# Kernel tuning notes

Measured on AMD Instinct MI355X. Metric: run time of the kernel, lower is better.

The kernel has to match this reference:

```python
import jax, jax.numpy as jnp
import numpy as np


def setup_inputs() -> dict:
    key = jax.random.key(0)
    k1, k2 = jax.random.split(key)
    B, N, G = 16, 200000, 128
    velocity = jax.random.normal(k1, (B, 3, G, G, G), dtype=jnp.float32)
    points = jax.random.uniform(k2, (B, N, 3), dtype=jnp.float32, minval=-2.5, maxval=2.5)
    bounding_box = jnp.array([[-2.5, 2.5], [-2.5, 2.5], [-2.5, 2.5]], dtype=jnp.float32)
    return {"velocity": velocity, "points": points, "bounding_box": bounding_box, "grid_size": G}


def reference(velocity, points, bounding_box, grid_size):
    # velocity: [B, 3, G, G, G]; points: [B, N, 3]; bounding_box: [3, 2]
    B, N, dim = points.shape
    G = grid_size
    # permute channels last and flatten grid, matching torch .permute(0,2,3,4,1).view(B,-1,3)
    vel = jnp.transpose(velocity, (0, 2, 3, 4, 1)).reshape(B, G * G * G, dim)
    bb = bounding_box
    # map points into continuous grid coordinates, per-axis
    uvw = (points - bb[:, 0]) / (bb[:, 1] - bb[:, 0]) * (G - 1)  # [B, N, 3]
    f1 = jnp.clip(jnp.floor(jax.lax.stop_gradient(uvw)), 0, G - 1)
    frac = uvw - f1          # fu, fv, fw
    gfrac = f1 + 1.0 - uvw   # gu, gv, gw
    i1 = f1.astype(jnp.int32)                      # floor indices (clamped)
    i2 = jnp.clip(i1 + 1, 0, G - 1)                # ceil indices (clamped)

    def gather(idx):  # idx: [B, N] -> [B, N, 3]
        return jax.vmap(lambda v, i: v[i])(vel, idx)

    out = jnp.zeros((B, N, dim), dtype=velocity.dtype)
    # 8 trilinear corners
    for iu, wu in ((i1[..., 0], gfrac[..., 0]), (i2[..., 0], frac[..., 0])):
        for iv, wv in ((i1[..., 1], gfrac[..., 1]), (i2[..., 1], frac[..., 1])):
            for iw, ww in ((i1[..., 2], gfrac[..., 2]), (i2[..., 2], frac[..., 2])):
                idx = (iu * G + iv) * G + iw
                out = out + gather(idx) * (wu * wv * ww)[..., None]
    return out
```

## Files before the change

kernel.cpp:

```cpp
#include <hip/hip_runtime.h>
#include <hip/hip_fp16.h>


constexpr int G = 128;
constexpr long long G3 = (long long)G * G * G;
constexpr int NSLAB = 8;
constexpr int NBU = 32, NBV = 32;
constexpr int NBIN = NBU * NBV;
constexpr int WINPTS = 4096;
constexpr int NIT = WINPTS / 256;
constexpr int MAXWIN = 64;

__global__ __launch_bounds__(256) void bin_kernel(
    const float* __restrict__ pts,
    const float* __restrict__ bb,
    int* __restrict__ Pt,
    unsigned long long* __restrict__ payload,
    int N, int nwin)
{
    __shared__ int hist[NBIN];
    __shared__ int psum[256];

    int b = blockIdx.x / nwin;
    int w = blockIdx.x % nwin;
    for (int i = threadIdx.x; i < NBIN; i += 256) hist[i] = 0;
    __syncthreads();

    const float Gm1 = (float)(G - 1);
    float bx0 = bb[0], bx1 = bb[1];
    float by0 = bb[2], by1 = bb[3];
    float bz0 = bb[4], bz1 = bb[5];
    long long pbase = (long long)b * N;
    int n0 = w * WINPTS;

    unsigned long long qc[NIT];
    #pragma unroll
    for (int it = 0; it < NIT; ++it) {
        int n = n0 + it * 256 + threadIdx.x;
        qc[it] = ~0ull;
        if (n < N) {
            const float* p = pts + (pbase + n) * 3;
            float u  = (p[0] - bx0) / (bx1 - bx0) * Gm1;
            float v  = (p[1] - by0) / (by1 - by0) * Gm1;
            float wz = (p[2] - bz0) / (bz1 - bz0) * Gm1;
            u  = fminf(fmaxf(u, 0.f), Gm1);
            v  = fminf(fmaxf(v, 0.f), Gm1);
            wz = fminf(fmaxf(wz, 0.f), Gm1);
            unsigned int qu = (unsigned int)(u * 1024.0f);
            unsigned int qv = (unsigned int)(v * 1024.0f);
            unsigned int qw = (unsigned int)(wz * 1024.0f);
            int nl = n - n0;
            qc[it] = (unsigned long long)qu
                   | ((unsigned long long)qv << 17)
                   | ((unsigned long long)qw << 34)
                   | ((unsigned long long)nl << 51);
            atomicAdd(&hist[((qu >> 12) << 5) | (qv >> 12)], 1);
        }
    }
    __syncthreads();

    int t = threadIdx.x;
    int l0 = hist[4 * t], l1 = hist[4 * t + 1], l2 = hist[4 * t + 2], l3 = hist[4 * t + 3];
    int s = l0 + l1 + l2 + l3;
    psum[t] = s;
    __syncthreads();
    for (int off = 1; off < 256; off <<= 1) {
        int v = (t >= off) ? psum[t - off] : 0;
        __syncthreads();
        psum[t] += v;
        __syncthreads();
    }
    int run = psum[t] - s;

    long long prow = ((long long)b * NBIN + 4 * t) * nwin + w;
    Pt[prow]            = run; hist[4 * t]     = run; run += l0;
    Pt[prow + nwin]     = run; hist[4 * t + 1] = run; run += l1;
    Pt[prow + 2 * nwin] = run; hist[4 * t + 2] = run; run += l2;
    Pt[prow + 3 * nwin] = run; hist[4 * t + 3] = run; run += l3;
    __syncthreads();

    unsigned long long* seg = payload + (long long)(b * nwin + w) * WINPTS;
    #pragma unroll
    for (int it = 0; it < NIT; ++it) {
        unsigned long long q = qc[it];
        if (q != ~0ull) {
            unsigned int qu = (unsigned int)(q & 0x1FFFF);
            unsigned int qv = (unsigned int)((q >> 17) & 0x1FFFF);
            int bin = ((qu >> 12) << 5) | (qv >> 12);
            int pos = atomicAdd(&hist[bin], 1);
            seg[pos] = q;
        }
    }
}

__global__ __launch_bounds__(256) void trilerp_lds_kernel(
    const float* __restrict__ vel,
    const int* __restrict__ Pt,
    const unsigned long long* __restrict__ payload,
    float* __restrict__ out,
    int N, int nwin)
{
    __shared__ unsigned short s_h[3 * 25 * 128];
    __shared__ int loc[MAXWIN];
    __shared__ int sc[MAXWIN];

    int x = blockIdx.x;
    int slab = x & (NSLAB - 1);
    int rest = x >> 3;
    int b    = rest >> 7;
    int r2   = rest & 127;
    int iu4  = (slab << 2) | (r2 >> 5);
    int iv4  = r2 & 31;
    int binLocal = (iu4 << 5) | iv4;
    long long lin = (long long)b * NBIN + binLocal;

    int tid = threadIdx.x;
    if (tid < nwin) {
        int l  = Pt[lin * nwin + tid];
        int nl = (binLocal < NBIN - 1) ? Pt[(lin + 1) * nwin + tid]
                                       : min(WINPTS, N - tid * WINPTS);
        loc[tid] = l;
        sc[tid]  = nl - l;
    } else if (tid < MAXWIN) {
        loc[tid] = 0; sc[tid] = 0;
    }

    int u0 = iu4 << 2, v0 = iv4 << 2;
    for (int k = 0; k < 10; ++k) {
        int idx = tid + k * 256;
        if (idx < 2400) {
            int f4 = idx & 31;
            int ru = idx >> 5;
            int ch = ru / 25;
            int r  = ru - ch * 25;
            int gu = min(u0 + r / 5, G - 1);
            int gv = min(v0 + (r - (r / 5) * 5), G - 1);
            long long src = (((long long)b * 3 + ch) << 21) + ((long long)gu << 14) + (gv << 7) + (f4 << 2);
            float4 val = *reinterpret_cast<const float4*>(vel + src);
            unsigned int lo32 = (unsigned int)__half_as_ushort(__float2half(val.x))
                              | ((unsigned int)__half_as_ushort(__float2half(val.y)) << 16);
            unsigned int hi32 = (unsigned int)__half_as_ushort(__float2half(val.z))
                              | ((unsigned int)__half_as_ushort(__float2half(val.w)) << 16);
            *reinterpret_cast<uint2*>(&s_h[((ch * 25 + r) << 7) + (f4 << 2)]) = make_uint2(lo32, hi32);
        }
    }
    __syncthreads();

    for (int off = 1; off < MAXWIN; off <<= 1) {
        int v = 0;
        if (tid < MAXWIN && tid >= off) v = sc[tid - off];
        __syncthreads();
        if (tid < MAXWIN) sc[tid] += v;
        __syncthreads();
    }
    int total = sc[nwin - 1];
    const float Gm1 = (float)(G - 1);
    const float INV1024 = 1.0f / 1024.0f;

    auto h2f = [](unsigned short us) -> float {
        return __half2float(__ushort_as_half(us));
    };

    for (int i = tid; i < total; i += 256) {
        int lo2 = 0, hi2 = nwin - 1;
        while (lo2 < hi2) { int mid = (lo2 + hi2) >> 1; if (sc[mid] > i) hi2 = mid; else lo2 = mid + 1; }
        int w = lo2;
        int excl = (w == 0) ? 0 : sc[w - 1];
        long long pidx = (long long)(b * nwin + w) * WINPTS + loc[w] + (i - excl);
        unsigned long long q = payload[pidx];
        unsigned int qu = (unsigned int)(q & 0x1FFFF);
        unsigned int qv = (unsigned int)((q >> 17) & 0x1FFFF);
        unsigned int qw = (unsigned int)((q >> 34) & 0x1FFFF);
        int nl = (int)(q >> 51);
        int t = (int)((long long)b * N + w * WINPTS + nl);

        float u  = (float)qu * INV1024;
        float v  = (float)qv * INV1024;
        float wq = (float)qw * INV1024;

        float fu = floorf(u);
        float fv = floorf(v);
        float fw = floorf(wq);

        float du = u - fu, dv = v - fv, dw = wq - fw;
        float gu = fu + 1.0f - u;
        float gv = fv + 1.0f - v;
        float gw = fw + 1.0f - wq;

        int iu1 = (int)fu, iv1 = (int)fv, iw1 = (int)fw;
        int iu2 = min(iu1 + 1, G - 1);
        int iv2 = min(iv1 + 1, G - 1);
        int iwb = min(iw1, G - 2);
        bool lo = (iw1 <= G - 2);

        float w11 = gu * gv, w12 = gu * dv, w21 = du * gv, w22 = du * dv;

        int du1 = iu1 - u0, dv1 = iv1 - v0;
        int du2 = iu2 - u0, dv2 = iv2 - v0;

        float o[3];
        #pragma unroll
        for (int ch = 0; ch < 3; ++ch) {
            int rb = ch * 25;
            int b11 = (rb + du1 * 5 + dv1) << 7;
            int b12 = (rb + du1 * 5 + dv2) << 7;
            int b21 = (rb + du2 * 5 + dv1) << 7;
            int b22 = (rb + du2 * 5 + dv2) << 7;
            float l11 = h2f(s_h[b11 + iwb]), h11 = h2f(s_h[b11 + iwb + 1]);
            float l12 = h2f(s_h[b12 + iwb]), h12 = h2f(s_h[b12 + iwb + 1]);
            float l21 = h2f(s_h[b21 + iwb]), h21 = h2f(s_h[b21 + iwb + 1]);
            float l22 = h2f(s_h[b22 + iwb]), h22 = h2f(s_h[b22 + iwb + 1]);
            float a11 = lo ? l11 : h11;
            float a12 = lo ? l12 : h12;
            float a21 = lo ? l21 : h21;
            float a22 = lo ? l22 : h22;
            o[ch] = w11 * (gw * a11 + dw * h11)
                  + w12 * (gw * a12 + dw * h12)
                  + w21 * (gw * a21 + dw * h21)
                  + w22 * (gw * a22 + dw * h22);
        }

        float* op = out + (long long)t * 3;
        op[0] = o[0]; op[1] = o[1]; op[2] = o[2];
    }
}

__global__ __launch_bounds__(256) void trilerp_pair_kernel(
    const float* __restrict__ vel, const float* __restrict__ pts,
    const float* __restrict__ bb, float* __restrict__ out,
    int N, int nchunk)
{
    int bid  = blockIdx.x;
    int slab = bid & (NSLAB - 1);
    int t    = bid >> 3;
    int c    = t % nchunk;
    int b    = t / nchunk;
    int n = c * 256 + threadIdx.x;
    if (n >= N) return;

    float bx0 = bb[0], bx1 = bb[1];
    float by0 = bb[2], by1 = bb[3];
    float bz0 = bb[4], bz1 = bb[5];
    long long pi = (long long)b * N + n;
    const float* p = pts + pi * 3;
    float px = p[0], py = p[1], pz = p[2];
    const float Gm1 = (float)(G - 1);
    float u = (px - bx0) / (bx1 - bx0) * Gm1;
    float fu = fminf(fmaxf(floorf(u), 0.f), Gm1);
    int iu1 = (int)fu;
    if ((iu1 >> 4) != slab) return;
    float v = (py - by0) / (by1 - by0) * Gm1;
    float w = (pz - bz0) / (bz1 - bz0) * Gm1;
    float fv = fminf(fmaxf(floorf(v), 0.f), Gm1);
    float fw = fminf(fmaxf(floorf(w), 0.f), Gm1);
    float du = u - fu, dv = v - fv, dw = w - fw;
    float gu = fu + 1.0f - u, gv = fv + 1.0f - v, gw = fw + 1.0f - w;
    int iv1 = (int)fv, iw1 = (int)fw;
    int iu2 = min(iu1 + 1, G - 1);
    int iv2 = min(iv1 + 1, G - 1);
    int iwb = min(iw1, G - 2);
    bool lo = (iw1 <= G - 2);
    float w11 = gu * gv, w12 = gu * dv, w21 = du * gv, w22 = du * dv;
    const float* vb = vel + (long long)b * 3 * G3;
    long long o11 = (long long)((iu1 << 7) + iv1) * G + iwb;
    long long o12 = (long long)((iu1 << 7) + iv2) * G + iwb;
    long long o21 = (long long)((iu2 << 7) + iv1) * G + iwb;
    long long o22 = (long long)((iu2 << 7) + iv2) * G + iwb;
    float o[3];
    #pragma unroll
    for (int chn = 0; chn < 3; ++chn) {
        const float* vc = vb + (long long)chn * G3;
        float2 p11 = *reinterpret_cast<const float2*>(vc + o11);
        float2 p12 = *reinterpret_cast<const float2*>(vc + o12);
        float2 p21 = *reinterpret_cast<const float2*>(vc + o21);
        float2 p22 = *reinterpret_cast<const float2*>(vc + o22);
        float a11 = lo ? p11.x : p11.y;
        float a12 = lo ? p12.x : p12.y;
        float a21 = lo ? p21.x : p21.y;
        float a22 = lo ? p22.x : p22.y;
        o[chn] = w11 * (gw * a11 + dw * p11.y)
               + w12 * (gw * a12 + dw * p12.y)
               + w21 * (gw * a21 + dw * p21.y)
               + w22 * (gw * a22 + dw * p22.y);
    }
    float* op = out + pi * 3;
    op[0] = o[0]; op[1] = o[1]; op[2] = o[2];
}

extern "C" void kernel_launch(void* const* d_in, const int* in_sizes, int n_in,
                              void* d_out, int out_size, void* d_ws, size_t ws_size,
                              hipStream_t stream) {
    const float* vel = (const float*)d_in[0];
    const float* pts = (const float*)d_in[1];
    const float* bb  = (const float*)d_in[2];
    float* out = (float*)d_out;

    int B = (int)(in_sizes[0] / (3 * G3));
    int N = in_sizes[1] / (3 * B);
    int nwin = (N + WINPTS - 1) / WINPTS;

    auto align256 = [](size_t x) { return (x + 255) & ~(size_t)255; };
    size_t off_pt  = 0;
    size_t sz_pt   = (size_t)B * NBIN * nwin * 4;
    size_t off_pay = align256(off_pt + sz_pt);
    size_t sz_pay  = (size_t)B * nwin * WINPTS * 8;
    size_t need    = off_pay + sz_pay;

    if (ws_size >= need && nwin <= MAXWIN) {
        int* Pt = (int*)((char*)d_ws + off_pt);
        unsigned long long* payload = (unsigned long long*)((char*)d_ws + off_pay);

        bin_kernel<<<B * nwin, 256, 0, stream>>>(pts, bb, Pt, payload, N, nwin);
        trilerp_lds_kernel<<<B * NBIN, 256, 0, stream>>>(vel, Pt, payload, out, N, nwin);
    } else {
        int nchunk = (N + 255) / 256;
        long long blocks = (long long)B * nchunk * NSLAB;
        trilerp_pair_kernel<<<(int)blocks, 256, 0, stream>>>(vel, pts, bb, out, N, nchunk);
    }
}
```

Measured before the change: 165.8 us.

## Split spatial bins along w axis into two halves with smaller LDS tiles

```diff
diff --git a/kernel.cpp b/kernel.cpp
--- a/kernel.cpp
+++ b/kernel.cpp
@@ -5,11 +5,11 @@
 constexpr int G = 128;
 constexpr long long G3 = (long long)G * G * G;
 constexpr int NSLAB = 8;
-constexpr int NBU = 32, NBV = 32;
-constexpr int NBIN = NBU * NBV;
+constexpr int NBIN = 2048;
 constexpr int WINPTS = 4096;
 constexpr int NIT = WINPTS / 256;
 constexpr int MAXWIN = 64;
+constexpr int WROW = 68;
 
 __global__ __launch_bounds__(256) void bin_kernel(
     const float* __restrict__ pts,
@@ -54,14 +54,16 @@
                    | ((unsigned long long)qv << 17)
                    | ((unsigned long long)qw << 34)
                    | ((unsigned long long)nl << 51);
-            atomicAdd(&hist[((qu >> 12) << 5) | (qv >> 12)], 1);
+            int bin = ((qu >> 12) << 6) | (((qv >> 12)) << 1) | (qw >> 16);
+            atomicAdd(&hist[bin], 1);
         }
     }
     __syncthreads();
 
     int t = threadIdx.x;
-    int l0 = hist[4 * t], l1 = hist[4 * t + 1], l2 = hist[4 * t + 2], l3 = hist[4 * t + 3];
-    int s = l0 + l1 + l2 + l3;
+    int l[8], s = 0;
+    #pragma unroll
+    for (int j = 0; j < 8; ++j) { l[j] = hist[8 * t + j]; s += l[j]; }
     psum[t] = s;
     __syncthreads();
     for (int off = 1; off < 256; off <<= 1) {
@@ -72,11 +74,13 @@
     }
     int run = psum[t] - s;
 
-    long long prow = ((long long)b * NBIN + 4 * t) * nwin + w;
-    Pt[prow]            = run; hist[4 * t]     = run; run += l0;
-    Pt[prow + nwin]     = run; hist[4 * t + 1] = run; run += l1;
-    Pt[prow + 2 * nwin] = run; hist[4 * t + 2] = run; run += l2;
-    Pt[prow + 3 * nwin] = run; hist[4 * t + 3] = run; run += l3;
+    long long prow = ((long long)b * NBIN + 8 * t) * nwin + w;
+    #pragma unroll
+    for (int j = 0; j < 8; ++j) {
+        Pt[prow + (long long)j * nwin] = run;
+        hist[8 * t + j] = run;
+        run += l[j];
+    }
     __syncthreads();
 
     unsigned long long* seg = payload + (long long)(b * nwin + w) * WINPTS;
@@ -86,32 +90,34 @@
         if (q != ~0ull) {
             unsigned int qu = (unsigned int)(q & 0x1FFFF);
             unsigned int qv = (unsigned int)((q >> 17) & 0x1FFFF);
-            int bin = ((qu >> 12) << 5) | (qv >> 12);
+            unsigned int qw = (unsigned int)((q >> 34) & 0x1FFFF);
+            int bin = ((qu >> 12) << 6) | (((qv >> 12)) << 1) | (qw >> 16);
             int pos = atomicAdd(&hist[bin], 1);
             seg[pos] = q;
         }
     }
 }
 
-__global__ __launch_bounds__(256) void trilerp_lds_kernel(
+__global__ __launch_bounds__(128) void trilerp_lds_kernel(
     const float* __restrict__ vel,
     const int* __restrict__ Pt,
     const unsigned long long* __restrict__ payload,
     float* __restrict__ out,
     int N, int nwin)
 {
-    __shared__ unsigned short s_h[3 * 25 * 128];
+    __shared__ unsigned short s_h[3 * 25 * WROW];
     __shared__ int loc[MAXWIN];
     __shared__ int sc[MAXWIN];
 
     int x = blockIdx.x;
     int slab = x & (NSLAB - 1);
     int rest = x >> 3;
-    int b    = rest >> 7;
-    int r2   = rest & 127;
-    int iu4  = (slab << 2) | (r2 >> 5);
-    int iv4  = r2 & 31;
-    int binLocal = (iu4 << 5) | iv4;
+    int wh   = rest & 1;
+    int iv4  = (rest >> 1) & 31;
+    int j    = (rest >> 6) & 3;
+    int b    = rest >> 8;
+    int iu4  = (slab << 2) | j;
+    int binLocal = (iu4 << 6) | (iv4 << 1) | wh;
     long long lin = (long long)b * NBIN + binLocal;
 
     int tid = threadIdx.x;
@@ -126,22 +132,23 @@
     }
 
     int u0 = iu4 << 2, v0 = iv4 << 2;
+    int wb = wh * 60;
     for (int k = 0; k < 10; ++k) {
-        int idx = tid + k * 256;
-        if (idx < 2400) {
-            int f4 = idx & 31;
-            int ru = idx >> 5;
+        int idx = tid + k * 128;
+        if (idx < 1275) {
+            int f4 = idx % 17;
+            int ru = idx / 17;
             int ch = ru / 25;
             int r  = ru - ch * 25;
             int gu = min(u0 + r / 5, G - 1);
             int gv = min(v0 + (r - (r / 5) * 5), G - 1);
-            long long src = (((long long)b * 3 + ch) << 21) + ((long long)gu << 14) + (gv << 7) + (f4 << 2);
+            long long src = (((long long)b * 3 + ch) << 21) + ((long long)gu << 14) + (gv << 7) + wb + (f4 << 2);
             float4 val = *reinterpret_cast<const float4*>(vel + src);
             unsigned int lo32 = (unsigned int)__half_as_ushort(__float2half(val.x))
                               | ((unsigned int)__half_as_ushort(__float2half(val.y)) << 16);
             unsigned int hi32 = (unsigned int)__half_as_ushort(__float2half(val.z))
                               | ((unsigned int)__half_as_ushort(__float2half(val.w)) << 16);
-            *reinterpret_cast<uint2*>(&s_h[((ch * 25 + r) << 7) + (f4 << 2)]) = make_uint2(lo32, hi32);
+            *reinterpret_cast<uint2*>(&s_h[(ch * 25 + r) * WROW + (f4 << 2)]) = make_uint2(lo32, hi32);
         }
     }
     __syncthreads();
@@ -154,14 +161,13 @@
         __syncthreads();
     }
     int total = sc[nwin - 1];
-    const float Gm1 = (float)(G - 1);
     const float INV1024 = 1.0f / 1024.0f;
 
     auto h2f = [](unsigned short us) -> float {
         return __half2float(__ushort_as_half(us));
     };
 
-    for (int i = tid; i < total; i += 256) {
+    for (int i = tid; i < total; i += 128) {
         int lo2 = 0, hi2 = nwin - 1;
         while (lo2 < hi2) { int mid = (lo2 + hi2) >> 1; if (sc[mid] > i) hi2 = mid; else lo2 = mid + 1; }
         int w = lo2;
@@ -197,19 +203,20 @@
 
         int du1 = iu1 - u0, dv1 = iv1 - v0;
         int du2 = iu2 - u0, dv2 = iv2 - v0;
+        int wl = iwb - wb;
 
         float o[3];
         #pragma unroll
         for (int ch = 0; ch < 3; ++ch) {
             int rb = ch * 25;
-            int b11 = (rb + du1 * 5 + dv1) << 7;
-            int b12 = (rb + du1 * 5 + dv2) << 7;
-            int b21 = (rb + du2 * 5 + dv1) << 7;
-            int b22 = (rb + du2 * 5 + dv2) << 7;
-            float l11 = h2f(s_h[b11 + iwb]), h11 = h2f(s_h[b11 + iwb + 1]);
-            float l12 = h2f(s_h[b12 + iwb]), h12 = h2f(s_h[b12 + iwb + 1]);
-            float l21 = h2f(s_h[b21 + iwb]), h21 = h2f(s_h[b21 + iwb + 1]);
-            float l22 = h2f(s_h[b22 + iwb]), h22 = h2f(s_h[b22 + iwb + 1]);
+            int b11 = (rb + du1 * 5 + dv1) * WROW + wl;
+            int b12 = (rb + du1 * 5 + dv2) * WROW + wl;
+            int b21 = (rb + du2 * 5 + dv1) * WROW + wl;
+            int b22 = (rb + du2 * 5 + dv2) * WROW + wl;
+            float l11 = h2f(s_h[b11]), h11 = h2f(s_h[b11 + 1]);
+            float l12 = h2f(s_h[b12]), h12 = h2f(s_h[b12 + 1]);
+            float l21 = h2f(s_h[b21]), h21 = h2f(s_h[b21 + 1]);
+            float l22 = h2f(s_h[b22]), h22 = h2f(s_h[b22 + 1]);
             float a11 = lo ? l11 : h11;
             float a12 = lo ? l12 : h12;
             float a21 = lo ? l21 : h21;
@@ -311,7 +318,7 @@
         unsigned long long* payload = (unsigned long long*)((char*)d_ws + off_pay);
 
         bin_kernel<<<B * nwin, 256, 0, stream>>>(pts, bb, Pt, payload, N, nwin);
-        trilerp_lds_kernel<<<B * NBIN, 256, 0, stream>>>(vel, Pt, payload, out, N, nwin);
+        trilerp_lds_kernel<<<B * NBIN, 128, 0, stream>>>(vel, Pt, payload, out, N, nwin);
     } else {
         int nchunk = (N + 255) / 256;
         long long blocks = (long long)B * nchunk * NSLAB;
```

Result: slower. 194.5 us (+17.3%).
